# Kernel optimization log

Hardware: AMD Instinct MI355X
Metric: run time of the kernel (lower is better)

## Reference

```python
import jax, jax.numpy as jnp
import numpy as np

N = 100000      # nodes
E = 1600000     # edges (avg degree 16)
F_N, F_E, H = 5, 3, 64
L = 3           # num GCN layers


def setup_inputs() -> dict:
    key = jax.random.key(0)
    ks = jax.random.split(key, 20)
    s = 0.05
    p = lambda k, shape: jax.random.normal(k, shape, jnp.float32) * s
    return {
        "x": jax.random.normal(ks[0], (N, F_N), jnp.float32),
        "edge_index": jax.random.randint(ks[1], (2, E), 0, N, dtype=jnp.int32),
        "edge_attr": jax.random.normal(ks[2], (E, F_E), jnp.float32),
        # node / edge encoders
        "Wn": p(ks[3], (F_N, H)), "bn": jnp.zeros((H,), jnp.float32),
        "We": p(ks[4], (F_E, H)), "be": jnp.zeros((H,), jnp.float32),
        # stacked GCNConv weights [L, H, H] and biases [L, H]
        "Wc": p(ks[5], (L, H, H)), "bc": jnp.zeros((L, H), jnp.float32),
        # demand forecast head
        "Wd1": p(ks[6], (H, H // 2)), "bd1": jnp.zeros((H // 2,), jnp.float32),
        "Wd2": p(ks[7], (H // 2, 1)), "bd2": jnp.zeros((1,), jnp.float32),
        # inventory optimizer head
        "Wi1": p(ks[8], (H, H // 2)), "bi1": jnp.zeros((H // 2,), jnp.float32),
        "Wi2": p(ks[9], (H // 2, 1)), "bi2": jnp.zeros((1,), jnp.float32),
    }


def reference(x, edge_index, edge_attr, Wn, bn, We, be, Wc, bc,
              Wd1, bd1, Wd2, bd2, Wi1, bi1, Wi2, bi2):
    src, dst = edge_index[0], edge_index[1]
    n = x.shape[0]

    h = jax.nn.relu(x @ Wn + bn)                      # [N, H]
    _ea = jax.nn.relu(edge_attr @ We + be)            # encoded edge feats (GCNConv ignores them)

    # GCN symmetric normalization with self-loops: deg[i] = in_degree(i) + 1
    ones_e = jnp.ones(src.shape[0], h.dtype)
    deg = jax.ops.segment_sum(ones_e, dst, num_segments=n) + 1.0
    dinv = jax.lax.rsqrt(deg)                         # [N]
    norm_e = dinv[src] * dinv[dst]                    # [E]
    norm_self = (dinv * dinv)[:, None]                # [N, 1]

    for l in range(Wc.shape[0]):
        hw = h @ Wc[l]                                # [N, H]
        msgs = norm_e[:, None] * hw[src]              # gather + scale, [E, H]
        agg = jax.ops.segment_sum(msgs, dst, num_segments=n) + norm_self * hw
        h = jax.nn.relu(agg + bc[l])

    demand = jax.nn.relu(h @ Wd1 + bd1) @ Wd2 + bd2   # [N, 1]
    inventory = jax.nn.relu(h @ Wi1 + bi1) @ Wi2 + bi2
    return demand, inventory
```

## Files before the change

### kernel.cpp

```cpp
#include <hip/hip_runtime.h>

#define H 64
#define FN 5
#define EPB 4096
#define BSHIFT 8
#define CAP2 4864

typedef _Float16 half4 __attribute__((ext_vector_type(4)));
typedef _Float16 half8 __attribute__((ext_vector_type(8)));
typedef float    float8v __attribute__((ext_vector_type(8)));

__global__ void k_bscatter2(const int* __restrict__ src, const int* __restrict__ dst,
                            int* __restrict__ lofs_g, int* __restrict__ bcounts,
                            int* __restrict__ binned, int nE, int nbB) {
    __shared__ int lh[512], lpos[512], lcur[512], tmp[256];
    __shared__ int stage[EPB];
    int t = threadIdx.x;
    int e0 = blockIdx.x * EPB;
    int es[16], ed[16];
    lh[t] = 0; lh[t + 256] = 0;
    __syncthreads();
#pragma unroll
    for (int i = 0; i < 16; ++i) {
        int e = e0 + i * 256 + t;
        bool v = e < nE;
        es[i] = v ? src[e] : 0;
        ed[i] = v ? dst[e] : -1;
        if (v) atomicAdd(&lh[ed[i] >> BSHIFT], 1);
    }
    __syncthreads();
    int a0 = lh[2 * t], a1 = lh[2 * t + 1];
    tmp[t] = a0 + a1;
    __syncthreads();
    for (int s = 1; s < 256; s <<= 1) {
        int a = (t >= s) ? tmp[t - s] : 0;
        __syncthreads();
        tmp[t] += a;
        __syncthreads();
    }
    int ex = tmp[t] - (a0 + a1);
    lpos[2 * t] = ex;
    lpos[2 * t + 1] = ex + a0;
    __syncthreads();
    lcur[t] = lpos[t]; lcur[t + 256] = lpos[t + 256];
    size_t row = (size_t)blockIdx.x * (nbB + 1);
    for (int b = t; b <= nbB; b += 256) lofs_g[row + b] = lpos[b];
    for (int b = t; b < nbB; b += 256) if (lh[b]) atomicAdd(&bcounts[b], lh[b]);
    __syncthreads();
#pragma unroll
    for (int i = 0; i < 16; ++i) {
        if (ed[i] >= 0) {
            int b = ed[i] >> BSHIFT;
            int p = atomicAdd(&lcur[b], 1);
            stage[p] = es[i] | ((ed[i] & 255) << 17);
        }
    }
    __syncthreads();
    int total = lpos[nbB];
    for (int j = t; j < total; j += 256) binned[e0 + j] = stage[j];
}

__global__ void k_bscan2(const int* __restrict__ bcounts, int* __restrict__ bbase, int nbB) {
    __shared__ int tmp[512];
    int t = threadIdx.x;
    int v = (t < nbB) ? bcounts[t] : 0;
    tmp[t] = v;
    __syncthreads();
    for (int s = 1; s < 512; s <<= 1) {
        int a = (t >= s) ? tmp[t - s] : 0;
        __syncthreads();
        tmp[t] += a;
        __syncthreads();
    }
    if (t < nbB) bbase[t + 1] = tmp[t];
    if (t == 0) bbase[0] = 0;
}

__global__ void k_bcsr2(const int* __restrict__ binned, const int* __restrict__ lofs_g,
                        const int* __restrict__ bbase, int* __restrict__ row_ptr,
                        int* __restrict__ csr_src, float* __restrict__ dinv,
                        int n, int nE, int nbE, int nbB) {
    __shared__ int len_s[512], start_s[512], roff[512], tmp[256];
    __shared__ int deg[256], st[256], cur[256];
    __shared__ int lbuf[CAP2];
    __shared__ int stage2[CAP2];
    int t = threadIdx.x;
    int B = blockIdx.x;
    int node0 = B << BSHIFT;
    int nn = min(256, n - node0);
    len_s[t] = 0; len_s[t + 256] = 0;
    __syncthreads();
    for (int sb = t; sb < nbE; sb += 256) {
        size_t row = (size_t)sb * (nbB + 1);
        int o0 = lofs_g[row + B], o1 = lofs_g[row + B + 1];
        len_s[sb] = o1 - o0;
        start_s[sb] = sb * EPB + o0;
    }
    __syncthreads();
    int a0 = len_s[2 * t], a1 = len_s[2 * t + 1];
    tmp[t] = a0 + a1;
    __syncthreads();
    for (int s = 1; s < 256; s <<= 1) {
        int a = (t >= s) ? tmp[t - s] : 0;
        __syncthreads();
        tmp[t] += a;
        __syncthreads();
    }
    int ex = tmp[t] - (a0 + a1);
    roff[2 * t] = ex;
    roff[2 * t + 1] = ex + a0;
    __syncthreads();
    int total = min(roff[511] + len_s[511], CAP2);
    for (int sb = t; sb < nbE; sb += 256) {
        int s0 = start_s[sb], ln = len_s[sb], d0 = roff[sb];
        for (int k = 0; k < ln; ++k) {
            int d = d0 + k;
            if (d < CAP2) lbuf[d] = binned[s0 + k];
        }
    }
    deg[t] = 0;
    __syncthreads();
    for (int i = t; i < total; i += 256) atomicAdd(&deg[(lbuf[i] >> 17) & 255], 1);
    __syncthreads();
    tmp[t] = deg[t];
    __syncthreads();
    for (int s = 1; s < 256; s <<= 1) {
        int a = (t >= s) ? tmp[t - s] : 0;
        __syncthreads();
        tmp[t] += a;
        __syncthreads();
    }
    st[t] = tmp[t] - deg[t];
    cur[t] = st[t];
    __syncthreads();
    int base = bbase[B];
    if (t < nn) {
        row_ptr[node0 + t] = base + st[t];
        dinv[node0 + t] = 1.0f / sqrtf((float)deg[t] + 1.0f);
    }
    if (B == 0 && t == 0) row_ptr[n] = nE;
    for (int i = t; i < total; i += 256) {
        int p0 = lbuf[i];
        int p = atomicAdd(&cur[(p0 >> 17) & 255], 1);
        int sv = p0 & 0x1FFFF;
        if (p < CAP2) stage2[p] = sv;
        else csr_src[base + p] = sv;
    }
    __syncthreads();
    for (int i = t; i < total; i += 256) csr_src[base + i] = stage2[i];
}

__global__ void k_enc(const float* __restrict__ x, const float* __restrict__ Wn,
                      const float* __restrict__ bn, const float* __restrict__ dinv,
                      _Float16* __restrict__ g0, int n) {
    int tid = blockIdx.x * 256 + threadIdx.x;
    int node = tid >> 6, ch = tid & 63;
    if (node >= n) return;
    float acc = bn[ch];
#pragma unroll
    for (int k = 0; k < FN; ++k)
        acc += x[(size_t)node * FN + k] * Wn[k * H + ch];
    g0[(size_t)node * H + ch] = (_Float16)(fmaxf(acc, 0.f) * dinv[node]);
}

__global__ void k_layer(const _Float16* __restrict__ gin, const int* __restrict__ csr_src,
                        const int* __restrict__ row_ptr, const float* __restrict__ dinv,
                        const float* __restrict__ W, const float* __restrict__ bias,
                        _Float16* __restrict__ gout, float* __restrict__ hout,
                        int n, int last) {
    __shared__ float As[64 * 68];
    __shared__ int rp_s[65];
    __shared__ float dv_s[64];
    int t = threadIdx.x;
    int wave = t >> 6, lane = t & 63;
    int base = blockIdx.x * 64;
    if (t < 65) rp_s[t] = row_ptr[min(base + t, n)];
    if (t >= 128 && t < 192) {
        int nd = base + (t - 128);
        dv_s[t - 128] = (nd < n) ? dinv[nd] : 0.f;
    }
    __syncthreads();

    int c8 = (lane >> 3) * 8;
    int slot = lane & 7;
    for (int it = 0; it < 8; ++it) {
        int rA = it * 8 + wave, rB = rA + 4;
        int nodeA = base + rA, nodeB = base + rB;
        float8v accA = 0.f, accB = 0.f;
        int iA = rp_s[rA], eA = rp_s[rA + 1];
        int iB = rp_s[rB], eB = rp_s[rB + 1];
        int cA = (eA - iA) >> 3, cB = (eB - iB) >> 3;
        int xA = 0, xB = 0, txA = 0, txB = 0;
        int tbA = iA + (cA << 3), tbB = iB + (cB << 3);
        bool tvA = (tbA + slot < eA), tvB = (tbB + slot < eB);
        if (cA) xA = csr_src[iA + slot];
        if (cB) xB = csr_src[iB + slot];
        if (tvA) txA = csr_src[tbA + slot];
        if (tvB) txB = csr_src[tbB + slot];
        while (cA && cB) {
            half8 vA = *(const half8*)(gin + (size_t)xA * H + c8);
            half8 vB = *(const half8*)(gin + (size_t)xB * H + c8);
            iA += 8; iB += 8; --cA; --cB;
            if (cA) xA = csr_src[iA + slot];
            if (cB) xB = csr_src[iB + slot];
#pragma unroll
            for (int k = 0; k < 8; ++k) { accA[k] += (float)vA[k]; accB[k] += (float)vB[k]; }
        }
        while (cA) {
            half8 vA = *(const half8*)(gin + (size_t)xA * H + c8);
            iA += 8; --cA;
            if (cA) xA = csr_src[iA + slot];
#pragma unroll
            for (int k = 0; k < 8; ++k) accA[k] += (float)vA[k];
        }
        while (cB) {
            half8 vB = *(const half8*)(gin + (size_t)xB * H + c8);
            iB += 8; --cB;
            if (cB) xB = csr_src[iB + slot];
#pragma unroll
            for (int k = 0; k < 8; ++k) accB[k] += (float)vB[k];
        }
        if (tvA) {
            half8 vA = *(const half8*)(gin + (size_t)txA * H + c8);
#pragma unroll
            for (int k = 0; k < 8; ++k) accA[k] += (float)vA[k];
        }
        if (tvB) {
            half8 vB = *(const half8*)(gin + (size_t)txB * H + c8);
#pragma unroll
            for (int k = 0; k < 8; ++k) accB[k] += (float)vB[k];
        }
#pragma unroll
        for (int m = 1; m <= 4; m <<= 1) {
#pragma unroll
            for (int k = 0; k < 8; ++k) {
                accA[k] += __shfl_xor(accA[k], m, 64);
                accB[k] += __shfl_xor(accB[k], m, 64);
            }
        }
        if (slot == 0) {
            float oA[8], oB[8];
            if (nodeA < n) {
                half8 sA = *(const half8*)(gin + (size_t)nodeA * H + c8);
                float dA = dv_s[rA];
#pragma unroll
                for (int k = 0; k < 8; ++k) oA[k] = (accA[k] + (float)sA[k]) * dA;
            } else {
#pragma unroll
                for (int k = 0; k < 8; ++k) oA[k] = 0.f;
            }
            if (nodeB < n) {
                half8 sB = *(const half8*)(gin + (size_t)nodeB * H + c8);
                float dB = dv_s[rB];
#pragma unroll
                for (int k = 0; k < 8; ++k) oB[k] = (accB[k] + (float)sB[k]) * dB;
            } else {
#pragma unroll
                for (int k = 0; k < 8; ++k) oB[k] = 0.f;
            }
            *(float4*)&As[rA * 68 + c8]     = make_float4(oA[0], oA[1], oA[2], oA[3]);
            *(float4*)&As[rA * 68 + c8 + 4] = make_float4(oA[4], oA[5], oA[6], oA[7]);
            *(float4*)&As[rB * 68 + c8]     = make_float4(oB[0], oB[1], oB[2], oB[3]);
            *(float4*)&As[rB * 68 + c8 + 4] = make_float4(oB[4], oB[5], oB[6], oB[7]);
        }
    }
    __syncthreads();

    int tx = t & 15, ty = t >> 4;
    int c0 = tx * 4;
    const float* a0 = As + (ty * 4 + 0) * 68;
    const float* a1 = As + (ty * 4 + 1) * 68;
    const float* a2 = As + (ty * 4 + 2) * 68;
    const float* a3 = As + (ty * 4 + 3) * 68;
    float4 acc0 = make_float4(0.f, 0.f, 0.f, 0.f);
    float4 acc1 = acc0, acc2 = acc0, acc3 = acc0;
#pragma unroll 16
    for (int k = 0; k < H; ++k) {
        float4 w = *(const float4*)(W + k * H + c0);
        float v0 = a0[k], v1 = a1[k], v2 = a2[k], v3 = a3[k];
        acc0.x += v0 * w.x; acc0.y += v0 * w.y; acc0.z += v0 * w.z; acc0.w += v0 * w.w;
        acc1.x += v1 * w.x; acc1.y += v1 * w.y; acc1.z += v1 * w.z; acc1.w += v1 * w.w;
        acc2.x += v2 * w.x; acc2.y += v2 * w.y; acc2.z += v2 * w.z; acc2.w += v2 * w.w;
        acc3.x += v3 * w.x; acc3.y += v3 * w.y; acc3.z += v3 * w.z; acc3.w += v3 * w.w;
    }
    float4 b = *(const float4*)(bias + c0);
    float4 accs[4] = {acc0, acc1, acc2, acc3};
#pragma unroll
    for (int rr = 0; rr < 4; ++rr) {
        int r = ty * 4 + rr;
        int row = base + r;
        if (row < n) {
            float4 o;
            o.x = fmaxf(accs[rr].x + b.x, 0.f);
            o.y = fmaxf(accs[rr].y + b.y, 0.f);
            o.z = fmaxf(accs[rr].z + b.z, 0.f);
            o.w = fmaxf(accs[rr].w + b.w, 0.f);
            if (last) {
                *(float4*)(hout + (size_t)row * H + c0) = o;
            } else {
                float d = dv_s[r];
                half4 hh;
                hh.x = (_Float16)(o.x * d);
                hh.y = (_Float16)(o.y * d);
                hh.z = (_Float16)(o.z * d);
                hh.w = (_Float16)(o.w * d);
                *(half4*)(gout + (size_t)row * H + c0) = hh;
            }
        }
    }
}

__global__ void k_heads(const float* __restrict__ h,
                        const float* __restrict__ Wd1, const float* __restrict__ bd1,
                        const float* __restrict__ Wd2, const float* __restrict__ bd2,
                        const float* __restrict__ Wi1, const float* __restrict__ bi1,
                        const float* __restrict__ Wi2, const float* __restrict__ bi2,
                        float* __restrict__ out, int n) {
    __shared__ float hs[64 * 65];
    int lane = threadIdx.x;
    int base = blockIdx.x * 64;
    for (int r = 0; r < 64; ++r) {
        int row = base + r;
        hs[r * 65 + lane] = (row < n) ? h[(size_t)row * H + lane] : 0.f;
    }
    __syncthreads();

    float accd[32], acci[32];
#pragma unroll
    for (int j = 0; j < 32; ++j) { accd[j] = bd1[j]; acci[j] = bi1[j]; }
    for (int k = 0; k < H; ++k) {
        float hk = hs[lane * 65 + k];
#pragma unroll
        for (int j = 0; j < 32; ++j) {
            accd[j] += hk * Wd1[k * 32 + j];
            acci[j] += hk * Wi1[k * 32 + j];
        }
    }
    float demand = bd2[0], inventory = bi2[0];
#pragma unroll
    for (int j = 0; j < 32; ++j) {
        demand    += fmaxf(accd[j], 0.f) * Wd2[j];
        inventory += fmaxf(acci[j], 0.f) * Wi2[j];
    }
    int node = base + lane;
    if (node < n) {
        out[node] = demand;
        out[n + node] = inventory;
    }
}

extern "C" void kernel_launch(void* const* d_in, const int* in_sizes, int n_in,
                              void* d_out, int out_size, void* d_ws, size_t ws_size,
                              hipStream_t stream) {
    const float* x   = (const float*)d_in[0];
    const int*   ei  = (const int*)  d_in[1];
    const float* Wn  = (const float*)d_in[3];
    const float* bn  = (const float*)d_in[4];
    const float* Wc  = (const float*)d_in[7];
    const float* bc  = (const float*)d_in[8];
    const float* Wd1 = (const float*)d_in[9];
    const float* bd1 = (const float*)d_in[10];
    const float* Wd2 = (const float*)d_in[11];
    const float* bd2 = (const float*)d_in[12];
    const float* Wi1 = (const float*)d_in[13];
    const float* bi1 = (const float*)d_in[14];
    const float* Wi2 = (const float*)d_in[15];
    const float* bi2 = (const float*)d_in[16];

    const int n  = in_sizes[0] / FN;
    const int nE = in_sizes[1] / 2;
    const int* src = ei;
    const int* dst = ei + nE;

    const int nbE = (nE + EPB - 1) / EPB;
    const int nbB = (n + 255) >> BSHIFT;
    const int nbL = (n + 63) / 64;

    char* w = (char*)d_ws;
    int* binned    = (int*)w;   w += (size_t)nbE * EPB * 4;
    int* csr_src   = (int*)w;   w += (size_t)nE * 4;
    int* row_ptr   = (int*)w;   w += (size_t)(n + 4) * 4;
    float* dinv    = (float*)w; w += (size_t)n * 4;
    int* lofs      = (int*)w;   w += (size_t)nbE * (nbB + 1) * 4;
    int* bcounts   = (int*)w;   w += 512 * 4;
    int* bbase     = (int*)w;   w += 516 * 4;
    float* hbuf    = (float*)w; w += (size_t)n * H * 4;
    _Float16* gA   = (_Float16*)w; w += (size_t)n * H * 2;
    _Float16* gB   = (_Float16*)w; w += (size_t)n * H * 2;

    hipMemsetAsync(bcounts, 0, 512 * 4, stream);

    k_bscatter2<<<nbE, 256, 0, stream>>>(src, dst, lofs, bcounts, binned, nE, nbB);
    k_bscan2   <<<1,   512, 0, stream>>>(bcounts, bbase, nbB);
    k_bcsr2    <<<nbB, 256, 0, stream>>>(binned, lofs, bbase, row_ptr, csr_src,
                                         dinv, n, nE, nbE, nbB);

    k_enc<<<((size_t)n * 64 + 255) / 256, 256, 0, stream>>>(x, Wn, bn, dinv, gA, n);

    k_layer<<<nbL, 256, 0, stream>>>(gA, csr_src, row_ptr, dinv, Wc,
                                     bc, gB, hbuf, n, 0);
    k_layer<<<nbL, 256, 0, stream>>>(gB, csr_src, row_ptr, dinv, Wc + (size_t)H * H,
                                     bc + H, gA, hbuf, n, 0);
    k_layer<<<nbL, 256, 0, stream>>>(gA, csr_src, row_ptr, dinv, Wc + (size_t)2 * H * H,
                                     bc + 2 * H, gB, hbuf, n, 1);

    k_heads<<<(n + 63) / 64, 64, 0, stream>>>(hbuf, Wd1, bd1, Wd2, bd2,
                                              Wi1, bi1, Wi2, bi2, (float*)d_out, n);
}
```

Baseline: 379.7 us.

## Transpose bin offset table and parallelize CSR gather via binary search

Stores the per-block bin offsets transposed so each CSR-building block reads its column contiguously, and replaces the per-source-block serial copy loop with a flat per-element loop that uses a binary search over prefix offsets. It also makes the encoder process four nodes per thread with weights held in registers. The aim is to remove strided offset reads and the load imbalance of serial copies in CSR construction, at the cost of a 9-step binary search per edge.

Result: no change. 378.7 us (-0.3%).

```diff
diff --git a/kernel.cpp b/kernel.cpp
--- a/kernel.cpp
+++ b/kernel.cpp
@@ -11,8 +11,8 @@
 typedef float    float8v __attribute__((ext_vector_type(8)));
 
 __global__ void k_bscatter2(const int* __restrict__ src, const int* __restrict__ dst,
-                            int* __restrict__ lofs_g, int* __restrict__ bcounts,
-                            int* __restrict__ binned, int nE, int nbB) {
+                            int* __restrict__ lofs_t, int* __restrict__ bcounts,
+                            int* __restrict__ binned, int nE, int nbB, int nbE) {
     __shared__ int lh[512], lpos[512], lcur[512], tmp[256];
     __shared__ int stage[EPB];
     int t = threadIdx.x;
@@ -43,8 +43,7 @@
     lpos[2 * t + 1] = ex + a0;
     __syncthreads();
     lcur[t] = lpos[t]; lcur[t + 256] = lpos[t + 256];
-    size_t row = (size_t)blockIdx.x * (nbB + 1);
-    for (int b = t; b <= nbB; b += 256) lofs_g[row + b] = lpos[b];
+    for (int b = t; b <= nbB; b += 256) lofs_t[(size_t)b * nbE + blockIdx.x] = lpos[b];
     for (int b = t; b < nbB; b += 256) if (lh[b]) atomicAdd(&bcounts[b], lh[b]);
     __syncthreads();
 #pragma unroll
@@ -76,11 +75,11 @@
     if (t == 0) bbase[0] = 0;
 }
 
-__global__ void k_bcsr2(const int* __restrict__ binned, const int* __restrict__ lofs_g,
+__global__ void k_bcsr2(const int* __restrict__ binned, const int* __restrict__ lofs_t,
                         const int* __restrict__ bbase, int* __restrict__ row_ptr,
                         int* __restrict__ csr_src, float* __restrict__ dinv,
                         int n, int nE, int nbE, int nbB) {
-    __shared__ int len_s[512], start_s[512], roff[512], tmp[256];
+    __shared__ int start_s[512], roff[513], tmp[256];
     __shared__ int deg[256], st[256], cur[256];
     __shared__ int lbuf[CAP2];
     __shared__ int stage2[CAP2];
@@ -88,16 +87,18 @@
     int B = blockIdx.x;
     int node0 = B << BSHIFT;
     int nn = min(256, n - node0);
-    len_s[t] = 0; len_s[t + 256] = 0;
-    __syncthreads();
-    for (int sb = t; sb < nbE; sb += 256) {
-        size_t row = (size_t)sb * (nbB + 1);
-        int o0 = lofs_g[row + B], o1 = lofs_g[row + B + 1];
-        len_s[sb] = o1 - o0;
-        start_s[sb] = sb * EPB + o0;
-    }
-    __syncthreads();
-    int a0 = len_s[2 * t], a1 = len_s[2 * t + 1];
+    int s0i = 2 * t, s1i = 2 * t + 1;
+    int a0 = 0, a1 = 0;
+    if (s0i < nbE) {
+        int o0 = lofs_t[B * nbE + s0i], o1 = lofs_t[(B + 1) * nbE + s0i];
+        a0 = o1 - o0;
+        start_s[s0i] = s0i * EPB + o0;
+    } else start_s[s0i] = 0;
+    if (s1i < nbE) {
+        int o0 = lofs_t[B * nbE + s1i], o1 = lofs_t[(B + 1) * nbE + s1i];
+        a1 = o1 - o0;
+        start_s[s1i] = s1i * EPB + o0;
+    } else start_s[s1i] = 0;
     tmp[t] = a0 + a1;
     __syncthreads();
     for (int s = 1; s < 256; s <<= 1) {
@@ -109,14 +110,16 @@
     int ex = tmp[t] - (a0 + a1);
     roff[2 * t] = ex;
     roff[2 * t + 1] = ex + a0;
-    __syncthreads();
-    int total = min(roff[511] + len_s[511], CAP2);
-    for (int sb = t; sb < nbE; sb += 256) {
-        int s0 = start_s[sb], ln = len_s[sb], d0 = roff[sb];
-        for (int k = 0; k < ln; ++k) {
-            int d = d0 + k;
-            if (d < CAP2) lbuf[d] = binned[s0 + k];
-        }
+    if (t == 255) roff[512] = tmp[255];
+    __syncthreads();
+    int total = min(roff[512], CAP2);
+    for (int i = t; i < total; i += 256) {
+        int lo = 0, hi = 512;
+        while (hi - lo > 1) {
+            int mid = (lo + hi) >> 1;
+            if (roff[mid] <= i) lo = mid; else hi = mid;
+        }
+        lbuf[i] = binned[start_s[lo] + (i - roff[lo])];
     }
     deg[t] = 0;
     __syncthreads();
@@ -154,13 +157,24 @@
                       const float* __restrict__ bn, const float* __restrict__ dinv,
                       _Float16* __restrict__ g0, int n) {
     int tid = blockIdx.x * 256 + threadIdx.x;
-    int node = tid >> 6, ch = tid & 63;
-    if (node >= n) return;
-    float acc = bn[ch];
-#pragma unroll
-    for (int k = 0; k < FN; ++k)
-        acc += x[(size_t)node * FN + k] * Wn[k * H + ch];
-    g0[(size_t)node * H + ch] = (_Float16)(fmaxf(acc, 0.f) * dinv[node]);
+    int ch = threadIdx.x & 63;
+    int node0 = (tid >> 6) * 4;
+    if (node0 >= n) return;
+    float wr[FN];
+#pragma unroll
+    for (int k = 0; k < FN; ++k) wr[k] = Wn[k * H + ch];
+    float b = bn[ch];
+#pragma unroll
+    for (int j = 0; j < 4; ++j) {
+        int node = node0 + j;
+        if (node < n) {
+            float acc = b;
+#pragma unroll
+            for (int k = 0; k < FN; ++k)
+                acc += x[(size_t)node * FN + k] * wr[k];
+            g0[(size_t)node * H + ch] = (_Float16)(fmaxf(acc, 0.f) * dinv[node]);
+        }
+    }
 }
 
 __global__ void k_layer(const _Float16* __restrict__ gin, const int* __restrict__ csr_src,
@@ -381,7 +395,7 @@
     int* csr_src   = (int*)w;   w += (size_t)nE * 4;
     int* row_ptr   = (int*)w;   w += (size_t)(n + 4) * 4;
     float* dinv    = (float*)w; w += (size_t)n * 4;
-    int* lofs      = (int*)w;   w += (size_t)nbE * (nbB + 1) * 4;
+    int* lofs      = (int*)w;   w += (size_t)(nbB + 1) * nbE * 4;
     int* bcounts   = (int*)w;   w += 512 * 4;
     int* bbase     = (int*)w;   w += 516 * 4;
     float* hbuf    = (float*)w; w += (size_t)n * H * 4;
@@ -390,12 +404,12 @@
 
     hipMemsetAsync(bcounts, 0, 512 * 4, stream);
 
-    k_bscatter2<<<nbE, 256, 0, stream>>>(src, dst, lofs, bcounts, binned, nE, nbB);
+    k_bscatter2<<<nbE, 256, 0, stream>>>(src, dst, lofs, bcounts, binned, nE, nbB, nbE);
     k_bscan2   <<<1,   512, 0, stream>>>(bcounts, bbase, nbB);
     k_bcsr2    <<<nbB, 256, 0, stream>>>(binned, lofs, bbase, row_ptr, csr_src,
                                          dinv, n, nE, nbE, nbB);
 
-    k_enc<<<((size_t)n * 64 + 255) / 256, 256, 0, stream>>>(x, Wn, bn, dinv, gA, n);
+    k_enc<<<(n + 15) / 16, 256, 0, stream>>>(x, Wn, bn, dinv, gA, n);
 
     k_layer<<<nbL, 256, 0, stream>>>(gA, csr_src, row_ptr, dinv, Wc,
                                      bc, gB, hbuf, n, 0);
```
